# Kernel optimization log

Measured on AMD Instinct MI355X. Metric: run time of the kernel, lower is better.

## Reference

```python
import jax, jax.numpy as jnp
import numpy as np

N_TOKEN = 267735
HEAD = 20000
CUTOFFS = [20000, 20008, 20016, 200000, 267735]  # from cl_root_leaf_dict with 2 roots of 8 leaves
N_ROOTS = 2


def setup_inputs() -> dict:
    key = jax.random.key(0)
    k1, k2, k3, k4 = jax.random.split(key, 4)
    N, D = 1024, 1024
    hidden = jax.random.normal(k1, (N, D), dtype=jnp.float32)
    target = jax.random.randint(k2, (N,), 0, N_TOKEN)
    W = jax.random.normal(k3, (N_TOKEN, D), dtype=jnp.float32) * 0.02
    b = jnp.zeros((N_TOKEN,), dtype=jnp.float32)
    cluster_weight = jax.random.normal(k4, (2, D), dtype=jnp.float32) * 0.02
    cluster_bias = jnp.zeros((2,), dtype=jnp.float32)
    return {"hidden": hidden, "target": target, "W": W, "b": b,
            "cluster_weight": cluster_weight, "cluster_bias": cluster_bias}


def _nll(hidden, target, W, b, cw, cb):
    cutoff_ends = [0] + CUTOFFS
    # head = first 20000 vocab rows + 2 cluster rows (d_proj == d_embed -> no projection)
    head_w = jnp.concatenate([W[:HEAD], cw], axis=0)          # [20002, D]
    head_b = jnp.concatenate([b[:HEAD], cb], axis=0)          # [20002]
    head_lp = jax.nn.log_softmax(hidden @ head_w.T + head_b, axis=-1)  # [N, 20002]
    n_head_cols = head_lp.shape[1]
    rows = jnp.arange(hidden.shape[0])
    # segment 0: target in [0, 20000) -> nll directly from head log-probs
    lp0 = head_lp[rows, jnp.clip(target, 0, HEAD - 1)]
    nll = -lp0  # only valid where target < HEAD; overwritten below otherwise
    for i in range(1, len(CUTOFFS)):
        l, r = cutoff_ends[i], cutoff_ends[i + 1]
        # per-segment tail logits for all tokens (masked combine keeps shapes static)
        tail_lp = jax.nn.log_softmax(hidden @ W[l:r].T + b[l:r], axis=-1)  # [N, r-l]
        # routing column exactly as in the torch code:
        # j = i-1 for root segments, -(i - n_roots) for the two cluster segments
        j = (i - 1) if i <= N_ROOTS else (n_head_cols - (i - N_ROOTS))
        lp_i = head_lp[:, j] + tail_lp[rows, jnp.clip(target - l, 0, r - l - 1)]
        mask = (target >= l) & (target < r)
        nll = jnp.where(mask, -lp_i, nll)
    return nll


def reference(hidden, target, W, b, cluster_weight, cluster_bias):
    return _nll(hidden, target, W, b, cluster_weight, cluster_bias)
```

## Files before the change

### kernel.cpp

```cpp
#include <hip/hip_runtime.h>
#include <hip/hip_bf16.h>

#define D_DIM 1024
#define NTOK 267735
#define NEXT_ 267737
#define HEADN 20000

typedef __attribute__((ext_vector_type(8))) short bf16x8;
typedef __attribute__((ext_vector_type(4))) float f32x4;

__device__ __forceinline__ int seg_of(int c){
  if (c < HEADN)  return 0;
  if (c < 20008)  return 1;
  if (c < 20016)  return 2;
  if (c < 200000) return 3;
  if (c < NTOK)   return 4;
  return 0;
}

__device__ __forceinline__ unsigned pack2(float x, float y){
  __hip_bfloat16 a = __float2bfloat16(x);
  __hip_bfloat16 b = __float2bfloat16(y);
  unsigned short ua = *reinterpret_cast<unsigned short*>(&a);
  unsigned short ub = *reinterpret_cast<unsigned short*>(&b);
  return (unsigned)ua | ((unsigned)ub << 16);
}

#define BM 256
#define BN 128
#define BK 32
#define NTHREADS 512
#define NCOLT 2092
#define NBLK 8384

__device__ __forceinline__ int swz_w(int r, int k4){
  int c = (k4 >> 1) ^ ((r >> 1) & 3);
  return r*32 + c*8 + (k4 & 1)*4;
}
__device__ __forceinline__ int swz_r(int row, int q){
  return row*32 + ((q ^ ((row >> 1) & 3)) << 3);
}

__global__ __launch_bounds__(NTHREADS, 1) void gemm_lse_kernel(
    const float* __restrict__ hidden, const float* __restrict__ W,
    const float* __restrict__ bias,   const float* __restrict__ cw,
    const float* __restrict__ cb,     float* __restrict__ accg)
{
  const int b = blockIdx.x;
  const int k8 = b & 7;
  const int s  = b >> 3;
  const int xb = s & 3;
  const int yb = (s >> 2) * 8 + k8;
  if (yb >= NCOLT) return;

  __shared__ unsigned short lsA[BM * 32];
  __shared__ unsigned short lsB[BN * 32];

  const int tid = threadIdx.x;
  const int rowBase = xb * BM;
  const int colBase = yb * BN;

  const float* aSrc[4]; int aRow[4], aK4[4];
#pragma unroll
  for (int i=0;i<4;++i){
    int idx = tid + NTHREADS*i;
    aRow[i] = idx >> 3; aK4[i] = idx & 7;
    aSrc[i] = hidden + (size_t)(rowBase + aRow[i]) * D_DIM + aK4[i]*4;
  }
  const float* bSrc[2]; int bRow[2], bK4[2];
#pragma unroll
  for (int i=0;i<2;++i){
    int idx = tid + NTHREADS*i;
    bRow[i] = idx >> 3; bK4[i] = idx & 7;
    int c = colBase + bRow[i];
    const float* base;
    if (c < NTOK)       base = W  + (size_t)c * D_DIM;
    else if (c < NEXT_) base = cw + (size_t)(c - NTOK) * D_DIM;
    else                base = W;
    bSrc[i] = base + bK4[i]*4;
  }

  const int lane = tid & 63;
  const int wv = tid >> 6;
  const int wm = wv >> 1;
  const int wn = wv & 1;
  const int q  = lane >> 4;
  const int r16 = lane & 15;

  f32x4 acc[4][4];
#pragma unroll
  for (int i=0;i<4;++i)
#pragma unroll
    for (int j=0;j<4;++j) acc[i][j] = (f32x4){0.f,0.f,0.f,0.f};

  for (int kt = 0; kt < D_DIM/BK; ++kt){
    float4 av[4], bv[2];
#pragma unroll
    for (int i=0;i<4;++i) av[i] = *reinterpret_cast<const float4*>(aSrc[i] + kt*BK);
#pragma unroll
    for (int i=0;i<2;++i) bv[i] = *reinterpret_cast<const float4*>(bSrc[i] + kt*BK);
    __syncthreads();
#pragma unroll
    for (int i=0;i<4;++i){
      unsigned* p = reinterpret_cast<unsigned*>(&lsA[swz_w(aRow[i], aK4[i])]);
      p[0] = pack2(av[i].x, av[i].y); p[1] = pack2(av[i].z, av[i].w);
    }
#pragma unroll
    for (int i=0;i<2;++i){
      unsigned* p = reinterpret_cast<unsigned*>(&lsB[swz_w(bRow[i], bK4[i])]);
      p[0] = pack2(bv[i].x, bv[i].y); p[1] = pack2(bv[i].z, bv[i].w);
    }
    __syncthreads();
    bf16x8 afr[4], bfr[4];
#pragma unroll
    for (int f=0; f<4; ++f) afr[f] = *reinterpret_cast<const bf16x8*>(&lsA[swz_r(wm*64 + f*16 + r16, q)]);
#pragma unroll
    for (int f=0; f<4; ++f) bfr[f] = *reinterpret_cast<const bf16x8*>(&lsB[swz_r(wn*64 + f*16 + r16, q)]);
#pragma unroll
    for (int i=0;i<4;++i)
#pragma unroll
      for (int j=0;j<4;++j)
        acc[i][j] = __builtin_amdgcn_mfma_f32_16x16x32_bf16(afr[i], bfr[j], acc[i][j], 0, 0, 0);
  }

  int sq[4]; float bq[4];
#pragma unroll
  for (int f=0; f<4; ++f){
    int c = colBase + wn*64 + f*16 + r16;
    if (c < NTOK)       { sq[f] = seg_of(c); bq[f] = bias[c]; }
    else if (c < NEXT_) { sq[f] = 0;         bq[f] = cb[c - NTOK]; }
    else                { sq[f] = -1;        bq[f] = 0.f; }
  }
  int sfirst = seg_of(colBase);
  int clast  = colBase + BN - 1; if (clast > NEXT_-1) clast = NEXT_-1;
  int slast  = seg_of(clast);
  int smin = sfirst, smax = slast;
  if (slast < sfirst){ smin = 0; smax = 4; }

#pragma unroll
  for (int i=0;i<4;++i){
#pragma unroll
    for (int r=0;r<4;++r){
      float e[4];
#pragma unroll
      for (int f=0;f<4;++f) e[f] = __expf(acc[i][f][r] + bq[f]);
      int rowg = rowBase + wm*64 + i*16 + (lane>>4)*4 + r;
      for (int s2 = smin; s2 <= smax; ++s2){
        float p = 0.f;
#pragma unroll
        for (int f=0;f<4;++f) p += (sq[f]==s2) ? e[f] : 0.f;
#pragma unroll
        for (int off=1; off<16; off<<=1) p += __shfl_xor(p, off, 16);
        if ((lane & 15) == 0 && p != 0.f) atomicAdd(&accg[rowg*8 + s2], p);
      }
    }
  }
}

__global__ __launch_bounds__(256) void finalize_kernel(
    const float* __restrict__ hidden, const int* __restrict__ target,
    const float* __restrict__ W,      const float* __restrict__ bias,
    const float* __restrict__ cw,     const float* __restrict__ cb,
    const float* __restrict__ accg,   float* __restrict__ out)
{
  const int row  = blockIdx.x * 4 + (threadIdx.x >> 6);
  const int lane = threadIdx.x & 63;
  const int t = target[row];

  const float4* h4 = reinterpret_cast<const float4*>(hidden + (size_t)row * D_DIM);
  const float4* w1 = reinterpret_cast<const float4*>(W + (size_t)t * D_DIM);
  int s = 0; const float* jraw = W; float jb = 0.f;
  if (t >= HEADN){
    if      (t < 20008)  { s=1; jraw = W;          jb = bias[0]; }
    else if (t < 20016)  { s=2; jraw = W + D_DIM;  jb = bias[1]; }
    else if (t < 200000) { s=3; jraw = cw + D_DIM; jb = cb[1];   }
    else                 { s=4; jraw = cw;         jb = cb[0];   }
  }
  const float4* w2 = reinterpret_cast<const float4*>(jraw);

  float p1 = 0.f, p2 = 0.f;
#pragma unroll
  for (int j=0;j<4;++j){
    float4 hv = h4[lane + 64*j];
    float4 av = w1[lane + 64*j];
    float4 bv = w2[lane + 64*j];
    p1 += hv.x*av.x + hv.y*av.y + hv.z*av.z + hv.w*av.w;
    p2 += hv.x*bv.x + hv.y*bv.y + hv.z*bv.z + hv.w*bv.w;
  }
#pragma unroll
  for (int off=32; off; off>>=1){
    p1 += __shfl_xor(p1, off, 64);
    p2 += __shfl_xor(p2, off, 64);
  }

  if (lane == 0){
    float lseH = __logf(accg[row*8 + 0]);
    float nll;
    if (t < HEADN){
      nll = -(p1 + bias[t] - lseH);
    } else {
      float lseS = __logf(accg[row*8 + s]);
      nll = -((p2 + jb - lseH) + (p1 + bias[t] - lseS));
    }
    out[row] = nll;
  }
}

extern "C" void kernel_launch(void* const* d_in, const int* in_sizes, int n_in,
                              void* d_out, int out_size, void* d_ws, size_t ws_size,
                              hipStream_t stream)
{
  const float* hidden = (const float*)d_in[0];
  const int*   target = (const int*)  d_in[1];
  const float* W      = (const float*)d_in[2];
  const float* bias   = (const float*)d_in[3];
  const float* cw     = (const float*)d_in[4];
  const float* cb     = (const float*)d_in[5];
  float* out  = (float*)d_out;
  float* accg = (float*)d_ws;

  hipMemsetAsync(accg, 0, 1024*8*sizeof(float), stream);

  gemm_lse_kernel<<<NBLK, NTHREADS, 0, stream>>>(hidden, W, bias, cw, cb, accg);
  finalize_kernel<<<256, 256, 0, stream>>>(hidden, target, W, bias, cw, cb, accg, out);
}
```

Before: 929.7 us.

## Double-buffer LDS tiles and prefetch next K-slice during MFMA compute

Replaces the single shared-memory buffer with two ping-pong buffers. The global loads for the next K step are issued before the MFMA work on the current buffer, and the converted values are stored into the other buffer afterwards, so only one barrier is needed per step instead of two. This aims to hide global-load latency behind matrix math. It doubles LDS use to about 48KB per block and keeps more values live in registers, which could raise register pressure.

```diff
diff --git a/kernel.cpp b/kernel.cpp
--- a/kernel.cpp
+++ b/kernel.cpp
@@ -30,6 +30,7 @@
 #define BN 128
 #define BK 32
 #define NTHREADS 512
+#define KSTEPS (D_DIM/BK)
 #define NCOLT 2092
 #define NBLK 8384
 
@@ -48,13 +49,15 @@
 {
   const int b = blockIdx.x;
   const int k8 = b & 7;
-  const int s  = b >> 3;
-  const int xb = s & 3;
-  const int yb = (s >> 2) * 8 + k8;
+  const int sq_ = b >> 3;
+  const int xb = sq_ & 3;
+  const int yb = (sq_ >> 2) * 8 + k8;
   if (yb >= NCOLT) return;
 
-  __shared__ unsigned short lsA[BM * 32];
-  __shared__ unsigned short lsB[BN * 32];
+  __shared__ unsigned short lsA0[BM * 32];
+  __shared__ unsigned short lsB0[BN * 32];
+  __shared__ unsigned short lsA1[BM * 32];
+  __shared__ unsigned short lsB1[BN * 32];
 
   const int tid = threadIdx.x;
   const int rowBase = xb * BM;
@@ -87,40 +90,83 @@
   const int q  = lane >> 4;
   const int r16 = lane & 15;
 
+  int wA0 = swz_w(aRow[0], aK4[0]), wA1 = swz_w(aRow[1], aK4[1]);
+  int wA2 = swz_w(aRow[2], aK4[2]), wA3 = swz_w(aRow[3], aK4[3]);
+  int wB0 = swz_w(bRow[0], bK4[0]), wB1 = swz_w(bRow[1], bK4[1]);
+  int rA0 = swz_r(wm*64 +  0 + r16, q), rA1 = swz_r(wm*64 + 16 + r16, q);
+  int rA2 = swz_r(wm*64 + 32 + r16, q), rA3 = swz_r(wm*64 + 48 + r16, q);
+  int rB0 = swz_r(wn*64 +  0 + r16, q), rB1 = swz_r(wn*64 + 16 + r16, q);
+  int rB2 = swz_r(wn*64 + 32 + r16, q), rB3 = swz_r(wn*64 + 48 + r16, q);
+
   f32x4 acc[4][4];
 #pragma unroll
   for (int i=0;i<4;++i)
 #pragma unroll
     for (int j=0;j<4;++j) acc[i][j] = (f32x4){0.f,0.f,0.f,0.f};
 
-  for (int kt = 0; kt < D_DIM/BK; ++kt){
-    float4 av[4], bv[2];
-#pragma unroll
-    for (int i=0;i<4;++i) av[i] = *reinterpret_cast<const float4*>(aSrc[i] + kt*BK);
-#pragma unroll
-    for (int i=0;i<2;++i) bv[i] = *reinterpret_cast<const float4*>(bSrc[i] + kt*BK);
-    __syncthreads();
-#pragma unroll
-    for (int i=0;i<4;++i){
-      unsigned* p = reinterpret_cast<unsigned*>(&lsA[swz_w(aRow[i], aK4[i])]);
-      p[0] = pack2(av[i].x, av[i].y); p[1] = pack2(av[i].z, av[i].w);
-    }
-#pragma unroll
-    for (int i=0;i<2;++i){
-      unsigned* p = reinterpret_cast<unsigned*>(&lsB[swz_w(bRow[i], bK4[i])]);
-      p[0] = pack2(bv[i].x, bv[i].y); p[1] = pack2(bv[i].z, bv[i].w);
-    }
-    __syncthreads();
-    bf16x8 afr[4], bfr[4];
-#pragma unroll
-    for (int f=0; f<4; ++f) afr[f] = *reinterpret_cast<const bf16x8*>(&lsA[swz_r(wm*64 + f*16 + r16, q)]);
-#pragma unroll
-    for (int f=0; f<4; ++f) bfr[f] = *reinterpret_cast<const bf16x8*>(&lsB[swz_r(wn*64 + f*16 + r16, q)]);
-#pragma unroll
-    for (int i=0;i<4;++i)
-#pragma unroll
-      for (int j=0;j<4;++j)
-        acc[i][j] = __builtin_amdgcn_mfma_f32_16x16x32_bf16(afr[i], bfr[j], acc[i][j], 0, 0, 0);
+#define LOADS(kn) \
+    va0 = *reinterpret_cast<const float4*>(aSrc[0] + (kn)*BK); \
+    va1 = *reinterpret_cast<const float4*>(aSrc[1] + (kn)*BK); \
+    va2 = *reinterpret_cast<const float4*>(aSrc[2] + (kn)*BK); \
+    va3 = *reinterpret_cast<const float4*>(aSrc[3] + (kn)*BK); \
+    vb0 = *reinterpret_cast<const float4*>(bSrc[0] + (kn)*BK); \
+    vb1 = *reinterpret_cast<const float4*>(bSrc[1] + (kn)*BK);
+
+#define STORES(LA, LB) { \
+    unsigned* p; \
+    p = reinterpret_cast<unsigned*>(&LA[wA0]); p[0] = pack2(va0.x, va0.y); p[1] = pack2(va0.z, va0.w); \
+    p = reinterpret_cast<unsigned*>(&LA[wA1]); p[0] = pack2(va1.x, va1.y); p[1] = pack2(va1.z, va1.w); \
+    p = reinterpret_cast<unsigned*>(&LA[wA2]); p[0] = pack2(va2.x, va2.y); p[1] = pack2(va2.z, va2.w); \
+    p = reinterpret_cast<unsigned*>(&LA[wA3]); p[0] = pack2(va3.x, va3.y); p[1] = pack2(va3.z, va3.w); \
+    p = reinterpret_cast<unsigned*>(&LB[wB0]); p[0] = pack2(vb0.x, vb0.y); p[1] = pack2(vb0.z, vb0.w); \
+    p = reinterpret_cast<unsigned*>(&LB[wB1]); p[0] = pack2(vb1.x, vb1.y); p[1] = pack2(vb1.z, vb1.w); }
+
+#define FRAGS_MFMA(LA, LB) { \
+    bf16x8 af0 = *reinterpret_cast<const bf16x8*>(&LA[rA0]); \
+    bf16x8 af1 = *reinterpret_cast<const bf16x8*>(&LA[rA1]); \
+    bf16x8 af2 = *reinterpret_cast<const bf16x8*>(&LA[rA2]); \
+    bf16x8 af3 = *reinterpret_cast<const bf16x8*>(&LA[rA3]); \
+    bf16x8 bf0 = *reinterpret_cast<const bf16x8*>(&LB[rB0]); \
+    bf16x8 bf1 = *reinterpret_cast<const bf16x8*>(&LB[rB1]); \
+    bf16x8 bf2 = *reinterpret_cast<const bf16x8*>(&LB[rB2]); \
+    bf16x8 bf3 = *reinterpret_cast<const bf16x8*>(&LB[rB3]); \
+    acc[0][0] = __builtin_amdgcn_mfma_f32_16x16x32_bf16(af0, bf0, acc[0][0], 0,0,0); \
+    acc[0][1] = __builtin_amdgcn_mfma_f32_16x16x32_bf16(af0, bf1, acc[0][1], 0,0,0); \
+    acc[0][2] = __builtin_amdgcn_mfma_f32_16x16x32_bf16(af0, bf2, acc[0][2], 0,0,0); \
+    acc[0][3] = __builtin_amdgcn_mfma_f32_16x16x32_bf16(af0, bf3, acc[0][3], 0,0,0); \
+    acc[1][0] = __builtin_amdgcn_mfma_f32_16x16x32_bf16(af1, bf0, acc[1][0], 0,0,0); \
+    acc[1][1] = __builtin_amdgcn_mfma_f32_16x16x32_bf16(af1, bf1, acc[1][1], 0,0,0); \
+    acc[1][2] = __builtin_amdgcn_mfma_f32_16x16x32_bf16(af1, bf2, acc[1][2], 0,0,0); \
+    acc[1][3] = __builtin_amdgcn_mfma_f32_16x16x32_bf16(af1, bf3, acc[1][3], 0,0,0); \
+    acc[2][0] = __builtin_amdgcn_mfma_f32_16x16x32_bf16(af2, bf0, acc[2][0], 0,0,0); \
+    acc[2][1] = __builtin_amdgcn_mfma_f32_16x16x32_bf16(af2, bf1, acc[2][1], 0,0,0); \
+    acc[2][2] = __builtin_amdgcn_mfma_f32_16x16x32_bf16(af2, bf2, acc[2][2], 0,0,0); \
+    acc[2][3] = __builtin_amdgcn_mfma_f32_16x16x32_bf16(af2, bf3, acc[2][3], 0,0,0); \
+    acc[3][0] = __builtin_amdgcn_mfma_f32_16x16x32_bf16(af3, bf0, acc[3][0], 0,0,0); \
+    acc[3][1] = __builtin_amdgcn_mfma_f32_16x16x32_bf16(af3, bf1, acc[3][1], 0,0,0); \
+    acc[3][2] = __builtin_amdgcn_mfma_f32_16x16x32_bf16(af3, bf2, acc[3][2], 0,0,0); \
+    acc[3][3] = __builtin_amdgcn_mfma_f32_16x16x32_bf16(af3, bf3, acc[3][3], 0,0,0); }
+
+  float4 va0, va1, va2, va3, vb0, vb1;
+
+  LOADS(0);
+  STORES(lsA0, lsB0);
+  __syncthreads();
+
+  for (int kt2 = 0; kt2 < KSTEPS/2; ++kt2){
+    {
+      const int kn = 2*kt2 + 1;
+      LOADS(kn);
+      FRAGS_MFMA(lsA0, lsB0);
+      STORES(lsA1, lsB1);
+      __syncthreads();
+    }
+    {
+      const int kn = 2*kt2 + 2;
+      if (kn < KSTEPS){ LOADS(kn); }
+      FRAGS_MFMA(lsA1, lsB1);
+      if (kn < KSTEPS){ STORES(lsA0, lsB0); __syncthreads(); }
+    }
   }
 
   int sq[4]; float bq[4];
```

Measured after the change: 1.814 ms. 95.1% more time.

## Pre-convert hidden to bf16 MFMA layout and double-buffer W tiles in LDS

Applied to the files above, without the earlier changes.

A prep kernel converts hidden to bf16 once, stored in a fragment-ordered layout. The GEMM then reads A fragments straight from global memory instead of re-converting fp32 A through LDS in every one of the thousands of blocks. W tiles are now double-buffered in LDS with the next tile's load issued before the MFMAs, so there is one barrier per k-step instead of two. The old kernel is kept as a fallback when the workspace is too small. The risk is that direct global A loads, though L2-resident, add latency inside the inner loop.

```diff
diff --git a/kernel.cpp b/kernel.cpp
--- a/kernel.cpp
+++ b/kernel.cpp
@@ -30,8 +30,12 @@
 #define BN 128
 #define BK 32
 #define NTHREADS 512
+#define KSTEPS (D_DIM/BK)
 #define NCOLT 2092
 #define NBLK 8384
+
+#define APRIME_OFF 32768
+#define APRIME_BYTES (1024*1024*2)
 
 __device__ __forceinline__ int swz_w(int r, int k4){
   int c = (k4 >> 1) ^ ((r >> 1) & 3);
@@ -41,32 +45,38 @@
   return row*32 + ((q ^ ((row >> 1) & 3)) << 3);
 }
 
-__global__ __launch_bounds__(NTHREADS, 1) void gemm_lse_kernel(
-    const float* __restrict__ hidden, const float* __restrict__ W,
+__global__ void prep_convert(const float* __restrict__ hidden,
+                             unsigned short* __restrict__ Ap)
+{
+  int t = blockIdx.x * blockDim.x + threadIdx.x;
+  int r16 = t & 15, kc = (t >> 4) & 127, rb = t >> 11;
+  const float4* src = reinterpret_cast<const float4*>(hidden + ((size_t)(rb*16 + r16) * D_DIM + kc*8));
+  float4 x = src[0], y = src[1];
+  uint4 o;
+  o.x = pack2(x.x, x.y); o.y = pack2(x.z, x.w);
+  o.z = pack2(y.x, y.y); o.w = pack2(y.z, y.w);
+  reinterpret_cast<uint4*>(Ap)[t] = o;
+}
+
+__global__ __launch_bounds__(NTHREADS, 1) void gemm_lse_adir(
+    const unsigned short* __restrict__ Ap, const float* __restrict__ W,
     const float* __restrict__ bias,   const float* __restrict__ cw,
     const float* __restrict__ cb,     float* __restrict__ accg)
 {
   const int b = blockIdx.x;
   const int k8 = b & 7;
-  const int s  = b >> 3;
-  const int xb = s & 3;
-  const int yb = (s >> 2) * 8 + k8;
+  const int sq_ = b >> 3;
+  const int xb = sq_ & 3;
+  const int yb = (sq_ >> 2) * 8 + k8;
   if (yb >= NCOLT) return;
 
-  __shared__ unsigned short lsA[BM * 32];
-  __shared__ unsigned short lsB[BN * 32];
+  __shared__ unsigned short lsB0[BN * 32];
+  __shared__ unsigned short lsB1[BN * 32];
 
   const int tid = threadIdx.x;
   const int rowBase = xb * BM;
   const int colBase = yb * BN;
 
-  const float* aSrc[4]; int aRow[4], aK4[4];
-#pragma unroll
-  for (int i=0;i<4;++i){
-    int idx = tid + NTHREADS*i;
-    aRow[i] = idx >> 3; aK4[i] = idx & 7;
-    aSrc[i] = hidden + (size_t)(rowBase + aRow[i]) * D_DIM + aK4[i]*4;
-  }
   const float* bSrc[2]; int bRow[2], bK4[2];
 #pragma unroll
   for (int i=0;i<2;++i){
@@ -87,13 +97,164 @@
   const int q  = lane >> 4;
   const int r16 = lane & 15;
 
+  const int wB0 = swz_w(bRow[0], bK4[0]), wB1 = swz_w(bRow[1], bK4[1]);
+  const int rB0 = swz_r(wn*64 +  0 + r16, q), rB1 = swz_r(wn*64 + 16 + r16, q);
+  const int rB2 = swz_r(wn*64 + 32 + r16, q), rB3 = swz_r(wn*64 + 48 + r16, q);
+
+  const unsigned short* a0 = Ap + (size_t)(xb*16 + wm*4 + 0)*16384 + q*128 + r16*8;
+  const unsigned short* a1 = Ap + (size_t)(xb*16 + wm*4 + 1)*16384 + q*128 + r16*8;
+  const unsigned short* a2 = Ap + (size_t)(xb*16 + wm*4 + 2)*16384 + q*128 + r16*8;
+  const unsigned short* a3 = Ap + (size_t)(xb*16 + wm*4 + 3)*16384 + q*128 + r16*8;
+
   f32x4 acc[4][4];
 #pragma unroll
   for (int i=0;i<4;++i)
 #pragma unroll
     for (int j=0;j<4;++j) acc[i][j] = (f32x4){0.f,0.f,0.f,0.f};
 
-  for (int kt = 0; kt < D_DIM/BK; ++kt){
+  {
+    float4 v0 = *reinterpret_cast<const float4*>(bSrc[0]);
+    float4 v1 = *reinterpret_cast<const float4*>(bSrc[1]);
+    unsigned* p;
+    p = reinterpret_cast<unsigned*>(&lsB0[wB0]); p[0] = pack2(v0.x, v0.y); p[1] = pack2(v0.z, v0.w);
+    p = reinterpret_cast<unsigned*>(&lsB0[wB1]); p[0] = pack2(v1.x, v1.y); p[1] = pack2(v1.z, v1.w);
+  }
+  __syncthreads();
+
+#pragma unroll 2
+  for (int kt = 0; kt < KSTEPS; ++kt){
+    unsigned short* Lr = (kt & 1) ? lsB1 : lsB0;
+    unsigned short* Lw = (kt & 1) ? lsB0 : lsB1;
+    const bool havenext = (kt + 1 < KSTEPS);
+
+    float4 nb0, nb1;
+    if (havenext){
+      nb0 = *reinterpret_cast<const float4*>(bSrc[0] + (kt+1)*BK);
+      nb1 = *reinterpret_cast<const float4*>(bSrc[1] + (kt+1)*BK);
+    }
+
+    bf16x8 af0 = *reinterpret_cast<const bf16x8*>(a0 + kt*512);
+    bf16x8 af1 = *reinterpret_cast<const bf16x8*>(a1 + kt*512);
+    bf16x8 af2 = *reinterpret_cast<const bf16x8*>(a2 + kt*512);
+    bf16x8 af3 = *reinterpret_cast<const bf16x8*>(a3 + kt*512);
+
+    bf16x8 bf0 = *reinterpret_cast<const bf16x8*>(&Lr[rB0]);
+    bf16x8 bf1 = *reinterpret_cast<const bf16x8*>(&Lr[rB1]);
+    bf16x8 bf2 = *reinterpret_cast<const bf16x8*>(&Lr[rB2]);
+    bf16x8 bf3 = *reinterpret_cast<const bf16x8*>(&Lr[rB3]);
+
+    acc[0][0] = __builtin_amdgcn_mfma_f32_16x16x32_bf16(af0, bf0, acc[0][0], 0,0,0);
+    acc[0][1] = __builtin_amdgcn_mfma_f32_16x16x32_bf16(af0, bf1, acc[0][1], 0,0,0);
+    acc[0][2] = __builtin_amdgcn_mfma_f32_16x16x32_bf16(af0, bf2, acc[0][2], 0,0,0);
+    acc[0][3] = __builtin_amdgcn_mfma_f32_16x16x32_bf16(af0, bf3, acc[0][3], 0,0,0);
+    acc[1][0] = __builtin_amdgcn_mfma_f32_16x16x32_bf16(af1, bf0, acc[1][0], 0,0,0);
+    acc[1][1] = __builtin_amdgcn_mfma_f32_16x16x32_bf16(af1, bf1, acc[1][1], 0,0,0);
+    acc[1][2] = __builtin_amdgcn_mfma_f32_16x16x32_bf16(af1, bf2, acc[1][2], 0,0,0);
+    acc[1][3] = __builtin_amdgcn_mfma_f32_16x16x32_bf16(af1, bf3, acc[1][3], 0,0,0);
+    acc[2][0] = __builtin_amdgcn_mfma_f32_16x16x32_bf16(af2, bf0, acc[2][0], 0,0,0);
+    acc[2][1] = __builtin_amdgcn_mfma_f32_16x16x32_bf16(af2, bf1, acc[2][1], 0,0,0);
+    acc[2][2] = __builtin_amdgcn_mfma_f32_16x16x32_bf16(af2, bf2, acc[2][2], 0,0,0);
+    acc[2][3] = __builtin_amdgcn_mfma_f32_16x16x32_bf16(af2, bf3, acc[2][3], 0,0,0);
+    acc[3][0] = __builtin_amdgcn_mfma_f32_16x16x32_bf16(af3, bf0, acc[3][0], 0,0,0);
+    acc[3][1] = __builtin_amdgcn_mfma_f32_16x16x32_bf16(af3, bf1, acc[3][1], 0,0,0);
+    acc[3][2] = __builtin_amdgcn_mfma_f32_16x16x32_bf16(af3, bf2, acc[3][2], 0,0,0);
+    acc[3][3] = __builtin_amdgcn_mfma_f32_16x16x32_bf16(af3, bf3, acc[3][3], 0,0,0);
+
+    if (havenext){
+      unsigned* p;
+      p = reinterpret_cast<unsigned*>(&Lw[wB0]); p[0] = pack2(nb0.x, nb0.y); p[1] = pack2(nb0.z, nb0.w);
+      p = reinterpret_cast<unsigned*>(&Lw[wB1]); p[0] = pack2(nb1.x, nb1.y); p[1] = pack2(nb1.z, nb1.w);
+    }
+    __syncthreads();
+  }
+
+  int sq[4]; float bq[4];
+#pragma unroll
+  for (int f=0; f<4; ++f){
+    int c = colBase + wn*64 + f*16 + r16;
+    if (c < NTOK)       { sq[f] = seg_of(c); bq[f] = bias[c]; }
+    else if (c < NEXT_) { sq[f] = 0;         bq[f] = cb[c - NTOK]; }
+    else                { sq[f] = -1;        bq[f] = 0.f; }
+  }
+  int sfirst = seg_of(colBase);
+  int clast  = colBase + BN - 1; if (clast > NEXT_-1) clast = NEXT_-1;
+  int slast  = seg_of(clast);
+  int smin = sfirst, smax = slast;
+  if (slast < sfirst){ smin = 0; smax = 4; }
+
+#pragma unroll
+  for (int i=0;i<4;++i){
+#pragma unroll
+    for (int r=0;r<4;++r){
+      float e[4];
+#pragma unroll
+      for (int f=0;f<4;++f) e[f] = __expf(acc[i][f][r] + bq[f]);
+      int rowg = rowBase + wm*64 + i*16 + (lane>>4)*4 + r;
+      for (int s2 = smin; s2 <= smax; ++s2){
+        float p = 0.f;
+#pragma unroll
+        for (int f=0;f<4;++f) p += (sq[f]==s2) ? e[f] : 0.f;
+#pragma unroll
+        for (int off=1; off<16; off<<=1) p += __shfl_xor(p, off, 16);
+        if ((lane & 15) == 0 && p != 0.f) atomicAdd(&accg[rowg*8 + s2], p);
+      }
+    }
+  }
+}
+
+__global__ __launch_bounds__(NTHREADS, 1) void gemm_lse_fb(
+    const float* __restrict__ hidden, const float* __restrict__ W,
+    const float* __restrict__ bias,   const float* __restrict__ cw,
+    const float* __restrict__ cb,     float* __restrict__ accg)
+{
+  const int b = blockIdx.x;
+  const int k8 = b & 7;
+  const int sq_ = b >> 3;
+  const int xb = sq_ & 3;
+  const int yb = (sq_ >> 2) * 8 + k8;
+  if (yb >= NCOLT) return;
+
+  __shared__ unsigned short lsA[BM * 32];
+  __shared__ unsigned short lsB[BN * 32];
+
+  const int tid = threadIdx.x;
+  const int rowBase = xb * BM;
+  const int colBase = yb * BN;
+
+  const float* aSrc[4]; int aRow[4], aK4[4];
+#pragma unroll
+  for (int i=0;i<4;++i){
+    int idx = tid + NTHREADS*i;
+    aRow[i] = idx >> 3; aK4[i] = idx & 7;
+    aSrc[i] = hidden + (size_t)(rowBase + aRow[i]) * D_DIM + aK4[i]*4;
+  }
+  const float* bSrc[2]; int bRow[2], bK4[2];
+#pragma unroll
+  for (int i=0;i<2;++i){
+    int idx = tid + NTHREADS*i;
+    bRow[i] = idx >> 3; bK4[i] = idx & 7;
+    int c = colBase + bRow[i];
+    const float* base;
+    if (c < NTOK)       base = W  + (size_t)c * D_DIM;
+    else if (c < NEXT_) base = cw + (size_t)(c - NTOK) * D_DIM;
+    else                base = W;
+    bSrc[i] = base + bK4[i]*4;
+  }
+
+  const int lane = tid & 63;
+  const int wv = tid >> 6;
+  const int wm = wv >> 1;
+  const int wn = wv & 1;
+  const int q  = lane >> 4;
+  const int r16 = lane & 15;
+
+  f32x4 acc[4][4];
+#pragma unroll
+  for (int i=0;i<4;++i)
+#pragma unroll
+    for (int j=0;j<4;++j) acc[i][j] = (f32x4){0.f,0.f,0.f,0.f};
+
+  for (int kt = 0; kt < KSTEPS; ++kt){
     float4 av[4], bv[2];
 #pragma unroll
     for (int i=0;i<4;++i) av[i] = *reinterpret_cast<const float4*>(aSrc[i] + kt*BK);
@@ -221,6 +382,12 @@
 
   hipMemsetAsync(accg, 0, 1024*8*sizeof(float), stream);
 
-  gemm_lse_kernel<<<NBLK, NTHREADS, 0, stream>>>(hidden, W, bias, cw, cb, accg);
+  if (ws_size >= (size_t)APRIME_OFF + APRIME_BYTES){
+    unsigned short* Ap = (unsigned short*)((char*)d_ws + APRIME_OFF);
+    prep_convert<<<512, 256, 0, stream>>>(hidden, Ap);
+    gemm_lse_adir<<<NBLK, NTHREADS, 0, stream>>>(Ap, W, bias, cw, cb, accg);
+  } else {
+    gemm_lse_fb<<<NBLK, NTHREADS, 0, stream>>>(hidden, W, bias, cw, cb, accg);
+  }
   finalize_kernel<<<256, 256, 0, stream>>>(hidden, target, W, bias, cw, cb, accg, out);
 }
```

Measured after the change: 939.6 us. Within noise of the previous version (+1.1%).

## Pre-convert hidden to bf16 fragment layout and read A directly from global memory

Applied to the files above, without the earlier changes.

A new prep kernel converts the hidden activations to bf16 once per call and stores them in an MFMA-fragment-ordered layout. The GEMM then loads A fragments straight from global memory instead of converting and staging them through LDS, and double-buffers only the W tile in LDS with a single barrier per k-step. Tiles shrink to 128x64 with 256 threads and a launch bound allowing several blocks per CU, trading more blocks and more atomics for higher occupancy and less LDS traffic. A is now re-read from global or L2 by every column tile, and the activation conversion is done on device, not moved to the host.

```diff
diff --git a/kernel.cpp b/kernel.cpp
--- a/kernel.cpp
+++ b/kernel.cpp
@@ -26,12 +26,17 @@
   return (unsigned)ua | ((unsigned)ub << 16);
 }
 
-#define BM 256
-#define BN 128
+#define BM 128
+#define BN 64
 #define BK 32
-#define NTHREADS 512
-#define NCOLT 2092
-#define NBLK 8384
+#define NTHREADS 256
+#define KSTEPS (D_DIM/BK)
+#define NROWB 8
+#define NCOLT 4184
+#define NBLK (NROWB*NCOLT)
+
+#define APRIME_OFF 32768
+#define APRIME_BYTES (1024*1024*2)
 
 __device__ __forceinline__ int swz_w(int r, int k4){
   int c = (k4 >> 1) ^ ((r >> 1) & 3);
@@ -41,32 +46,38 @@
   return row*32 + ((q ^ ((row >> 1) & 3)) << 3);
 }
 
-__global__ __launch_bounds__(NTHREADS, 1) void gemm_lse_kernel(
-    const float* __restrict__ hidden, const float* __restrict__ W,
+__global__ void prep_convert(const float* __restrict__ hidden,
+                             unsigned short* __restrict__ Ap)
+{
+  int t = blockIdx.x * blockDim.x + threadIdx.x;
+  int r16 = t & 15, kc = (t >> 4) & 127, rb = t >> 11;
+  const float4* src = reinterpret_cast<const float4*>(hidden + ((size_t)(rb*16 + r16) * D_DIM + kc*8));
+  float4 x = src[0], y = src[1];
+  uint4 o;
+  o.x = pack2(x.x, x.y); o.y = pack2(x.z, x.w);
+  o.z = pack2(y.x, y.y); o.w = pack2(y.z, y.w);
+  reinterpret_cast<uint4*>(Ap)[t] = o;
+}
+
+__global__ __launch_bounds__(NTHREADS, 6) void gemm_lse_adir(
+    const unsigned short* __restrict__ Ap, const float* __restrict__ W,
     const float* __restrict__ bias,   const float* __restrict__ cw,
     const float* __restrict__ cb,     float* __restrict__ accg)
 {
   const int b = blockIdx.x;
   const int k8 = b & 7;
-  const int s  = b >> 3;
-  const int xb = s & 3;
-  const int yb = (s >> 2) * 8 + k8;
+  const int sq_ = b >> 3;
+  const int xb = sq_ & 7;
+  const int yb = (sq_ >> 3) * 8 + k8;
   if (yb >= NCOLT) return;
 
-  __shared__ unsigned short lsA[BM * 32];
-  __shared__ unsigned short lsB[BN * 32];
+  __shared__ unsigned short lsB0[BN * 32];
+  __shared__ unsigned short lsB1[BN * 32];
 
   const int tid = threadIdx.x;
   const int rowBase = xb * BM;
   const int colBase = yb * BN;
 
-  const float* aSrc[4]; int aRow[4], aK4[4];
-#pragma unroll
-  for (int i=0;i<4;++i){
-    int idx = tid + NTHREADS*i;
-    aRow[i] = idx >> 3; aK4[i] = idx & 7;
-    aSrc[i] = hidden + (size_t)(rowBase + aRow[i]) * D_DIM + aK4[i]*4;
-  }
   const float* bSrc[2]; int bRow[2], bK4[2];
 #pragma unroll
   for (int i=0;i<2;++i){
@@ -87,46 +98,57 @@
   const int q  = lane >> 4;
   const int r16 = lane & 15;
 
-  f32x4 acc[4][4];
-#pragma unroll
-  for (int i=0;i<4;++i)
-#pragma unroll
-    for (int j=0;j<4;++j) acc[i][j] = (f32x4){0.f,0.f,0.f,0.f};
-
-  for (int kt = 0; kt < D_DIM/BK; ++kt){
-    float4 av[4], bv[2];
-#pragma unroll
-    for (int i=0;i<4;++i) av[i] = *reinterpret_cast<const float4*>(aSrc[i] + kt*BK);
-#pragma unroll
-    for (int i=0;i<2;++i) bv[i] = *reinterpret_cast<const float4*>(bSrc[i] + kt*BK);
+  const int wB0 = swz_w(bRow[0], bK4[0]), wB1 = swz_w(bRow[1], bK4[1]);
+  const int rB0 = swz_r(wn*32 +  0 + r16, q), rB1 = swz_r(wn*32 + 16 + r16, q);
+
+  const unsigned short* aBase = Ap + (size_t)(xb*8 + wm*4)*16384 + q*128 + r16*8;
+
+  f32x4 acc[4][2];
+#pragma unroll
+  for (int i=0;i<4;++i){ acc[i][0] = (f32x4){0,0,0,0}; acc[i][1] = (f32x4){0,0,0,0}; }
+
+  {
+    float4 v0 = *reinterpret_cast<const float4*>(bSrc[0]);
+    float4 v1 = *reinterpret_cast<const float4*>(bSrc[1]);
+    unsigned* p;
+    p = reinterpret_cast<unsigned*>(&lsB0[wB0]); p[0] = pack2(v0.x, v0.y); p[1] = pack2(v0.z, v0.w);
+    p = reinterpret_cast<unsigned*>(&lsB0[wB1]); p[0] = pack2(v1.x, v1.y); p[1] = pack2(v1.z, v1.w);
+  }
+  __syncthreads();
+
+  for (int kt = 0; kt < KSTEPS; ++kt){
+    unsigned short* Lr = (kt & 1) ? lsB1 : lsB0;
+    unsigned short* Lw = (kt & 1) ? lsB0 : lsB1;
+    const bool havenext = (kt + 1 < KSTEPS);
+
+    float4 nb0, nb1;
+    if (havenext){
+      nb0 = *reinterpret_cast<const float4*>(bSrc[0] + (kt+1)*BK);
+      nb1 = *reinterpret_cast<const float4*>(bSrc[1] + (kt+1)*BK);
+    }
+
+    bf16x8 bf0 = *reinterpret_cast<const bf16x8*>(&Lr[rB0]);
+    bf16x8 bf1 = *reinterpret_cast<const bf16x8*>(&Lr[rB1]);
+
+#pragma unroll
+    for (int i=0;i<4;++i){
+      bf16x8 af = *reinterpret_cast<const bf16x8*>(aBase + i*16384 + kt*512);
+      acc[i][0] = __builtin_amdgcn_mfma_f32_16x16x32_bf16(af, bf0, acc[i][0], 0,0,0);
+      acc[i][1] = __builtin_amdgcn_mfma_f32_16x16x32_bf16(af, bf1, acc[i][1], 0,0,0);
+    }
+
+    if (havenext){
+      unsigned* p;
+      p = reinterpret_cast<unsigned*>(&Lw[wB0]); p[0] = pack2(nb0.x, nb0.y); p[1] = pack2(nb0.z, nb0.w);
+      p = reinterpret_cast<unsigned*>(&Lw[wB1]); p[0] = pack2(nb1.x, nb1.y); p[1] = pack2(nb1.z, nb1.w);
+    }
     __syncthreads();
-#pragma unroll
-    for (int i=0;i<4;++i){
-      unsigned* p = reinterpret_cast<unsigned*>(&lsA[swz_w(aRow[i], aK4[i])]);
-      p[0] = pack2(av[i].x, av[i].y); p[1] = pack2(av[i].z, av[i].w);
-    }
-#pragma unroll
-    for (int i=0;i<2;++i){
-      unsigned* p = reinterpret_cast<unsigned*>(&lsB[swz_w(bRow[i], bK4[i])]);
-      p[0] = pack2(bv[i].x, bv[i].y); p[1] = pack2(bv[i].z, bv[i].w);
-    }
-    __syncthreads();
-    bf16x8 afr[4], bfr[4];
-#pragma unroll
-    for (int f=0; f<4; ++f) afr[f] = *reinterpret_cast<const bf16x8*>(&lsA[swz_r(wm*64 + f*16 + r16, q)]);
-#pragma unroll
-    for (int f=0; f<4; ++f) bfr[f] = *reinterpret_cast<const bf16x8*>(&lsB[swz_r(wn*64 + f*16 + r16, q)]);
-#pragma unroll
-    for (int i=0;i<4;++i)
-#pragma unroll
-      for (int j=0;j<4;++j)
-        acc[i][j] = __builtin_amdgcn_mfma_f32_16x16x32_bf16(afr[i], bfr[j], acc[i][j], 0, 0, 0);
-  }
-
-  int sq[4]; float bq[4];
-#pragma unroll
-  for (int f=0; f<4; ++f){
-    int c = colBase + wn*64 + f*16 + r16;
+  }
+
+  int sq[2]; float bq[2];
+#pragma unroll
+  for (int f=0; f<2; ++f){
+    int c = colBase + wn*32 + f*16 + r16;
     if (c < NTOK)       { sq[f] = seg_of(c); bq[f] = bias[c]; }
     else if (c < NEXT_) { sq[f] = 0;         bq[f] = cb[c - NTOK]; }
     else                { sq[f] = -1;        bq[f] = 0.f; }
@@ -141,14 +163,11 @@
   for (int i=0;i<4;++i){
 #pragma unroll
     for (int r=0;r<4;++r){
-      float e[4];
-#pragma unroll
-      for (int f=0;f<4;++f) e[f] = __expf(acc[i][f][r] + bq[f]);
+      float e0 = __expf(acc[i][0][r] + bq[0]);
+      float e1 = __expf(acc[i][1][r] + bq[1]);
       int rowg = rowBase + wm*64 + i*16 + (lane>>4)*4 + r;
       for (int s2 = smin; s2 <= smax; ++s2){
-        float p = 0.f;
-#pragma unroll
-        for (int f=0;f<4;++f) p += (sq[f]==s2) ? e[f] : 0.f;
+        float p = ((sq[0]==s2) ? e0 : 0.f) + ((sq[1]==s2) ? e1 : 0.f);
 #pragma unroll
         for (int off=1; off<16; off<<=1) p += __shfl_xor(p, off, 16);
         if ((lane & 15) == 0 && p != 0.f) atomicAdd(&accg[rowg*8 + s2], p);
@@ -218,9 +237,11 @@
   const float* cb     = (const float*)d_in[5];
   float* out  = (float*)d_out;
   float* accg = (float*)d_ws;
+  unsigned short* Ap = (unsigned short*)((char*)d_ws + APRIME_OFF);
 
   hipMemsetAsync(accg, 0, 1024*8*sizeof(float), stream);
 
-  gemm_lse_kernel<<<NBLK, NTHREADS, 0, stream>>>(hidden, W, bias, cw, cb, accg);
+  prep_convert<<<512, 256, 0, stream>>>(hidden, Ap);
+  gemm_lse_adir<<<NBLK, NTHREADS, 0, stream>>>(Ap, W, bias, cw, cb, accg);
   finalize_kernel<<<256, 256, 0, stream>>>(hidden, target, W, bias, cw, cb, accg, out);
 }
```

Result: slower. 1.710 ms (+83.9%).
